# Performance work log

Hardware: AMD Instinct MI355X
Metric: run time of the kernel (lower is better)

Reference implementation:

```python
import jax, jax.numpy as jnp
import numpy as np

S, B, H = 2048, 2, 1024
NH = 16
HD = H // NH  # 64


def setup_inputs() -> dict:
    key = jax.random.key(0)
    k1, k2 = jax.random.split(key)
    hidden_states = jax.random.normal(k1, (S, B, H), dtype=jnp.float32)
    W_qkv = jax.random.normal(k2, (3 * H, H), dtype=jnp.float32) * (H ** -0.5)
    b_qkv = jnp.zeros((3 * H,), dtype=jnp.float32)
    return {"hidden_states": hidden_states, "W_qkv": W_qkv, "b_qkv": b_qkv}


def reference(hidden_states, W_qkv, b_qkv):
    s, b, h = hidden_states.shape
    # QKV projection: [S,B,3H] -> [S,B,NH,3*HD] -> split
    qkv = hidden_states @ W_qkv.T + b_qkv
    qkv = qkv.reshape(s, b, NH, 3 * HD)
    q, k, v = jnp.split(qkv, 3, axis=-1)  # each [S,B,NH,HD]
    norm_factor = HD ** -0.5
    # scores: [B,NH,Sq,Sk]
    scores = jnp.einsum('sbhd,tbhd->bhst', q, k) * norm_factor
    # Cumsum sequence-op (seq_op_in_fp32=True): cumsum over key dim, scaled by Sq^-0.5
    probs = jnp.cumsum(scores.astype(jnp.float32), axis=-1) * (s ** -0.5)
    probs = probs.astype(hidden_states.dtype)
    # PV: [B,NH,Sq,HD] -> seq-first [Sq,B,NH*HD]
    ctx = jnp.einsum('bhst,tbhd->sbhd', probs, v)
    return ctx.reshape(s, b, h)
```

## Files before the change

### kernel.cpp

```cpp
#include <hip/hip_runtime.h>

#define S 2048
#define B 2
#define H 1024
#define NH 16
#define HD 64
#define THREE_H 3072
#define ROWS (S*B)

typedef __attribute__((ext_vector_type(8))) short short8;
typedef __attribute__((ext_vector_type(4))) float f32x4;
typedef const __attribute__((address_space(1))) unsigned int* gptr_t;
typedef __attribute__((address_space(3))) unsigned int* lptr_t;

#define N8_A (ROWS * H / 8)
#define N8_W (THREE_H * H / 8)

__device__ __forceinline__ ushort f2bf(float f) {
    union { float f; unsigned u; } v; v.f = f;
    unsigned r = v.u + 0x7fffu + ((v.u >> 16) & 1u);
    return (ushort)(r >> 16);
}

__global__ void cast_both(const float* __restrict__ A, const float* __restrict__ W,
                          ushort* __restrict__ Ab, ushort* __restrict__ Wb) {
    int i = blockIdx.x * 256 + threadIdx.x;
    const float4* s4;
    ushort* dst;
    if (i < N8_A) { s4 = (const float4*)A; dst = Ab; }
    else if (i < N8_A + N8_W) { s4 = (const float4*)W; dst = Wb; i -= N8_A; }
    else return;
    float4 a = s4[2 * i], b = s4[2 * i + 1];
    short8 o;
    o[0] = f2bf(a.x); o[1] = f2bf(a.y); o[2] = f2bf(a.z); o[3] = f2bf(a.w);
    o[4] = f2bf(b.x); o[5] = f2bf(b.y); o[6] = f2bf(b.z); o[7] = f2bf(b.w);
    *(short8*)(dst + 8 * (size_t)i) = o;
}

__global__ __launch_bounds__(256) void qkv_gemm_mfma(const ushort* __restrict__ Abf,
                                                     const ushort* __restrict__ Wbf,
                                                     const float* __restrict__ bias,
                                                     ushort* __restrict__ Qb,
                                                     ushort* __restrict__ Kb,
                                                     float* __restrict__ Vf) {
    __shared__ ushort Abuf[128 * 32];
    __shared__ ushort Bbuf[128 * 32];
    const int tid = threadIdx.x;
    const int wave = tid >> 6, lane = tid & 63;
    const int wr = wave >> 1, wc = wave & 1;
    const int row0 = blockIdx.x * 128;
    const int col0 = blockIdx.y * 128;

    f32x4 acc[4][4] = {};

    const int lrow = lane >> 2;
    const int lk   = (lane & 3) * 8;

    for (int k0 = 0; k0 < H; k0 += 32) {
#pragma unroll
        for (int p = 0; p < 2; ++p) {
            int c = wave * 2 + p;
            int row = c * 16 + lrow;
            __builtin_amdgcn_global_load_lds(
                (gptr_t)&Abf[(size_t)(row0 + row) * H + k0 + lk],
                (lptr_t)&Abuf[c * 512 + lane * 8], 16, 0, 0);
            __builtin_amdgcn_global_load_lds(
                (gptr_t)&Wbf[(size_t)(col0 + row) * H + k0 + lk],
                (lptr_t)&Bbuf[c * 512 + lane * 8], 16, 0, 0);
        }
        __syncthreads();

        short8 af[4], bfr[4];
#pragma unroll
        for (int m = 0; m < 4; ++m) {
            int ar = wr * 64 + m * 16 + (lane & 15);
            af[m] = *(const short8*)&Abuf[ar * 32 + (lane >> 4) * 8];
            int br = wc * 64 + m * 16 + (lane & 15);
            bfr[m] = *(const short8*)&Bbuf[br * 32 + (lane >> 4) * 8];
        }
#pragma unroll
        for (int m = 0; m < 4; ++m)
#pragma unroll
            for (int n = 0; n < 4; ++n)
                acc[m][n] = __builtin_amdgcn_mfma_f32_16x16x32_bf16(af[m], bfr[n], acc[m][n], 0, 0, 0);
        __syncthreads();
    }

#pragma unroll
    for (int n = 0; n < 4; ++n) {
        int cbase = col0 + wc * 64 + n * 16;
        int h   = cbase / 192;
        int r3  = cbase % 192;
        int sel = r3 >> 6;
        int d   = (r3 & 63) + (lane & 15);
        float bv = bias[cbase + (lane & 15)];
#pragma unroll
        for (int m = 0; m < 4; ++m) {
            int rowb = row0 + wr * 64 + m * 16 + (lane >> 4) * 4;
#pragma unroll
            for (int j = 0; j < 4; ++j) {
                int r = rowb + j;
                int s = r >> 1, b = r & 1;
                size_t off = ((size_t)((b * NH + h) * S + s)) * HD + d;
                float val = acc[m][n][j] + bv;
                if (sel == 0)      Qb[off] = f2bf(val);
                else if (sel == 1) Kb[off] = f2bf(val);
                else               Vf[off] = val;
            }
        }
    }
}

__global__ void vsuf_chunksum(const float* __restrict__ Vf, float* __restrict__ csum) {
    int idx = blockIdx.x * 256 + threadIdx.x;
    int col = idx & 2047;
    int chunk = idx >> 11;
    const float* vp = Vf + ((size_t)(col >> 6) * S + chunk * 32) * HD + (col & 63);
    float s = 0.f;
#pragma unroll
    for (int t = 0; t < 32; ++t) s += vp[(size_t)t * HD];
    csum[idx] = s;
}

__global__ void vsuft_final(const float* __restrict__ Vf, const float* __restrict__ csum,
                            ushort* __restrict__ Vt) {
    int idx = blockIdx.x * 256 + threadIdx.x;
    int col = idx & 2047;
    int chunk = idx >> 11;
    int bh = col >> 6, d = col & 63;
    float acc = 0.f;
    for (int c = chunk + 1; c < 64; ++c) acc += csum[c * 2048 + col];
    const float* vp = Vf + ((size_t)bh * S + chunk * 32) * HD + d;
    ushort buf[32];
#pragma unroll
    for (int tt = 31; tt >= 0; --tt) {
        acc += vp[(size_t)tt * HD];
        buf[tt] = f2bf(acc);
    }
    ushort* op = Vt + ((size_t)bh * HD + d) * S + chunk * 32;
#pragma unroll
    for (int q = 0; q < 4; ++q) {
        short8 o;
#pragma unroll
        for (int k = 0; k < 8; ++k) o[k] = buf[q * 8 + k];
        *(short8*)(op + q * 8) = o;
    }
}

__global__ __launch_bounds__(256) void ktrans(const ushort* __restrict__ Kb,
                                              ushort* __restrict__ Kt) {
    __shared__ ushort Ks[64][72];
    const int bh = blockIdx.x;
    const int t0 = blockIdx.y * 64;
    const int tid = threadIdx.x;
    {
        const int tt = tid >> 2, part = (tid & 3) * 16;
        const ushort* src = Kb + ((size_t)bh * S + t0 + tt) * HD + part;
        *(short8*)&Ks[tt][part]     = *(const short8*)(src);
        *(short8*)&Ks[tt][part + 8] = *(const short8*)(src + 8);
    }
    __syncthreads();
    {
        const int d = tid >> 2, tq = (tid & 3) * 16;
        ushort tmp[16];
#pragma unroll
        for (int k = 0; k < 16; ++k) tmp[k] = Ks[tq + k][d];
        ushort* dst = Kt + ((size_t)bh * HD + d) * S + t0 + tq;
        short8 o0, o1;
#pragma unroll
        for (int k = 0; k < 8; ++k) { o0[k] = tmp[k]; o1[k] = tmp[8 + k]; }
        *(short8*)dst = o0;
        *(short8*)(dst + 8) = o1;
    }
}

__global__ __launch_bounds__(256) void kvm_mfma(const ushort* __restrict__ Kt,
                                                const ushort* __restrict__ Vt,
                                                float* __restrict__ Mpart) {
    const int bh = blockIdx.x, kb = blockIdx.y;
    const int tid = threadIdx.x, wave = tid >> 6, lane = tid & 63;
    const int slice = kb * 4 + wave;
    const ushort* Kp = Kt + (size_t)bh * HD * S;
    const ushort* Vp = Vt + (size_t)bh * HD * S;
    f32x4 acc[4][4] = {};
    const int il = lane & 15;
    const int tbase = slice * 128 + (lane >> 4) * 8;
#pragma unroll
    for (int ks = 0; ks < 4; ++ks) {
        const int t = tbase + ks * 32;
        short8 af[4], bfv[4];
#pragma unroll
        for (int m = 0; m < 4; ++m) af[m]  = *(const short8*)&Kp[(size_t)(m * 16 + il) * S + t];
#pragma unroll
        for (int n = 0; n < 4; ++n) bfv[n] = *(const short8*)&Vp[(size_t)(n * 16 + il) * S + t];
#pragma unroll
        for (int m = 0; m < 4; ++m)
#pragma unroll
            for (int n = 0; n < 4; ++n)
                acc[m][n] = __builtin_amdgcn_mfma_f32_16x16x32_bf16(af[m], bfv[n], acc[m][n], 0, 0, 0);
    }
    float* Mp = Mpart + ((size_t)slice * 32 + bh) * 4096;
#pragma unroll
    for (int m = 0; m < 4; ++m)
#pragma unroll
        for (int n = 0; n < 4; ++n)
#pragma unroll
            for (int j = 0; j < 4; ++j) {
                int i  = m * 16 + (lane >> 4) * 4 + j;
                int jj = n * 16 + il;
                Mp[i * 64 + jj] = acc[m][n][j];
            }
}

__global__ __launch_bounds__(256) void qm_mfma(const ushort* __restrict__ Qb,
                                               const float* __restrict__ Mpart,
                                               float* __restrict__ out) {
    __shared__ ushort Mt[64][72];
    const int bh = blockIdx.x, b = bh >> 4, h = bh & 15;
    const int tid = threadIdx.x;
    {
        const int i = tid >> 2, jq = (tid & 3) * 16;
        f32x4 s0 = {}, s1 = {}, s2 = {}, s3 = {};
#pragma unroll
        for (int sl = 0; sl < 16; ++sl) {
            const float* p = Mpart + ((size_t)sl * 32 + bh) * 4096 + i * 64 + jq;
            s0 += *(const f32x4*)(p);
            s1 += *(const f32x4*)(p + 4);
            s2 += *(const f32x4*)(p + 8);
            s3 += *(const f32x4*)(p + 12);
        }
#pragma unroll
        for (int k = 0; k < 4; ++k) {
            Mt[jq + 0  + k][i] = f2bf(s0[k]);
            Mt[jq + 4  + k][i] = f2bf(s1[k]);
            Mt[jq + 8  + k][i] = f2bf(s2[k]);
            Mt[jq + 12 + k][i] = f2bf(s3[k]);
        }
    }
    __syncthreads();
    const int wave = tid >> 6, lane = tid & 63;
    const int sl15 = lane & 15, koct = (lane >> 4) * 8;
    const int s0b = blockIdx.y * 256 + wave * 64;
    f32x4 acc[4][4] = {};
#pragma unroll
    for (int ks = 0; ks < 2; ++ks) {
        short8 af[4], bfv[4];
#pragma unroll
        for (int m = 0; m < 4; ++m) {
            int s = s0b + m * 16 + sl15;
            af[m] = *(const short8*)&Qb[((size_t)bh * S + s) * HD + ks * 32 + koct];
        }
#pragma unroll
        for (int n = 0; n < 4; ++n)
            bfv[n] = *(const short8*)&Mt[n * 16 + sl15][ks * 32 + koct];
#pragma unroll
        for (int m = 0; m < 4; ++m)
#pragma unroll
            for (int n = 0; n < 4; ++n)
                acc[m][n] = __builtin_amdgcn_mfma_f32_16x16x32_bf16(af[m], bfv[n], acc[m][n], 0, 0, 0);
    }
    const float scale = 0.125f * 0.02209708691207961f;
#pragma unroll
    for (int m = 0; m < 4; ++m)
#pragma unroll
        for (int n = 0; n < 4; ++n)
#pragma unroll
            for (int j = 0; j < 4; ++j) {
                int s = s0b + m * 16 + (lane >> 4) * 4 + j;
                int d = n * 16 + sl15;
                out[(size_t)(s * B + b) * H + h * 64 + d] = acc[m][n][j] * scale;
            }
}

extern "C" void kernel_launch(void* const* d_in, const int* in_sizes, int n_in,
                              void* d_out, int out_size, void* d_ws, size_t ws_size,
                              hipStream_t stream) {
    const float* hidden = (const float*)d_in[0];
    const float* W      = (const float*)d_in[1];
    const float* bias   = (const float*)d_in[2];
    float* out = (float*)d_out;

    float*  Vf    = (float*)d_ws;
    ushort* Qb    = (ushort*)(Vf + 4194304);
    ushort* Kb    = Qb + 4194304;
    ushort* Kt    = Kb + 4194304;
    ushort* Vt    = Kt + 4194304;
    float*  csum  = (float*)(Vt + 4194304);
    float*  Mpart = csum + 131072;
    ushort* Abf   = (ushort*)(Mpart + 2097152);
    ushort* Wbf   = Abf + 4194304;

    cast_both<<<(N8_A + N8_W + 255) / 256, 256, 0, stream>>>(hidden, W, Abf, Wbf);
    qkv_gemm_mfma<<<dim3(ROWS / 128, THREE_H / 128), 256, 0, stream>>>(Abf, Wbf, bias, Qb, Kb, Vf);
    vsuf_chunksum<<<512, 256, 0, stream>>>(Vf, csum);
    vsuft_final<<<512, 256, 0, stream>>>(Vf, csum, Vt);
    ktrans<<<dim3(32, 32), 256, 0, stream>>>(Kb, Kt);
    kvm_mfma<<<dim3(32, 4), 256, 0, stream>>>(Kt, Vt, Mpart);
    qm_mfma<<<dim3(32, 8), 256, 0, stream>>>(Qb, Mpart, out);
}
```

Measured before the change: 86.16 us.

## Fuse K/V transpose into QKV GEMM epilogue and keep V in bf16

```diff
diff --git a/kernel.cpp b/kernel.cpp
--- a/kernel.cpp
+++ b/kernel.cpp
@@ -20,6 +20,10 @@
     union { float f; unsigned u; } v; v.f = f;
     unsigned r = v.u + 0x7fffu + ((v.u >> 16) & 1u);
     return (ushort)(r >> 16);
+}
+__device__ __forceinline__ float bf2f(ushort u) {
+    union { unsigned u; float f; } v; v.u = ((unsigned)u) << 16;
+    return v.f;
 }
 
 __global__ void cast_both(const float* __restrict__ A, const float* __restrict__ W,
@@ -41,10 +45,11 @@
                                                      const ushort* __restrict__ Wbf,
                                                      const float* __restrict__ bias,
                                                      ushort* __restrict__ Qb,
-                                                     ushort* __restrict__ Kb,
-                                                     float* __restrict__ Vf) {
+                                                     ushort* __restrict__ Kt,
+                                                     ushort* __restrict__ Vraw) {
     __shared__ ushort Abuf[128 * 32];
     __shared__ ushort Bbuf[128 * 32];
+    __shared__ ushort Ct[64][136];
     const int tid = threadIdx.x;
     const int wave = tid >> 6, lane = tid & 63;
     const int wr = wave >> 1, wc = wave & 1;
@@ -86,91 +91,102 @@
         __syncthreads();
     }
 
-#pragma unroll
-    for (int n = 0; n < 4; ++n) {
-        int cbase = col0 + wc * 64 + n * 16;
-        int h   = cbase / 192;
-        int r3  = cbase % 192;
-        int sel = r3 >> 6;
-        int d   = (r3 & 63) + (lane & 15);
-        float bv = bias[cbase + (lane & 15)];
-#pragma unroll
-        for (int m = 0; m < 4; ++m) {
-            int rowb = row0 + wr * 64 + m * 16 + (lane >> 4) * 4;
-#pragma unroll
-            for (int j = 0; j < 4; ++j) {
-                int r = rowb + j;
-                int s = r >> 1, b = r & 1;
-                size_t off = ((size_t)((b * NH + h) * S + s)) * HD + d;
-                float val = acc[m][n][j] + bv;
-                if (sel == 0)      Qb[off] = f2bf(val);
-                else if (sel == 1) Kb[off] = f2bf(val);
-                else               Vf[off] = val;
-            }
-        }
-    }
-}
-
-__global__ void vsuf_chunksum(const float* __restrict__ Vf, float* __restrict__ csum) {
+    const int il = lane & 15, g = lane >> 4;
+    const int t_base = row0 >> 1;
+#pragma unroll
+    for (int sg = 0; sg < 2; ++sg) {
+        int cseg = col0 + sg * 64;
+        int h = cseg / 192, rem = cseg % 192;
+        int sel = rem >> 6;
+        if (sel == 0) {
+            if (wc == sg) {
+#pragma unroll
+                for (int n = 0; n < 4; ++n) {
+                    int d = n * 16 + il;
+                    float bv = bias[cseg + d];
+#pragma unroll
+                    for (int m = 0; m < 4; ++m) {
+                        int rowb = row0 + wr * 64 + m * 16 + g * 4;
+#pragma unroll
+                        for (int j = 0; j < 4; ++j) {
+                            int r = rowb + j;
+                            int s = r >> 1, b = r & 1;
+                            Qb[((size_t)((b * NH + h) * S + s)) * HD + d] =
+                                f2bf(acc[m][n][j] + bv);
+                        }
+                    }
+                }
+            }
+        } else {
+            ushort* dst = (sel == 1) ? Kt : Vraw;
+            __syncthreads();
+            if (wc == sg) {
+#pragma unroll
+                for (int n = 0; n < 4; ++n) {
+                    int c = n * 16 + il;
+                    float bv = bias[cseg + c];
+#pragma unroll
+                    for (int m = 0; m < 4; ++m) {
+                        int t0 = wr * 32 + m * 8 + g * 2;
+                        uint lo = (uint)f2bf(acc[m][n][0] + bv) |
+                                  ((uint)f2bf(acc[m][n][2] + bv) << 16);
+                        uint hi = (uint)f2bf(acc[m][n][1] + bv) |
+                                  ((uint)f2bf(acc[m][n][3] + bv) << 16);
+                        *(uint*)&Ct[c][t0]      = lo;
+                        *(uint*)&Ct[c][64 + t0] = hi;
+                    }
+                }
+            }
+            __syncthreads();
+            {
+                int c = tid >> 2, sub = tid & 3, b = sub >> 1, th = (sub & 1) * 32;
+                ushort* op = dst + ((size_t)((b * NH + h) * HD + c)) * S + t_base + th;
+                const ushort* sp = &Ct[c][b * 64 + th];
+#pragma unroll
+                for (int q = 0; q < 4; ++q)
+                    *(short8*)(op + q * 8) = *(const short8*)(sp + q * 8);
+            }
+        }
+    }
+}
+
+__global__ void vsuf_chunksum(const ushort* __restrict__ Vraw, float* __restrict__ csum) {
     int idx = blockIdx.x * 256 + threadIdx.x;
     int col = idx & 2047;
     int chunk = idx >> 11;
-    const float* vp = Vf + ((size_t)(col >> 6) * S + chunk * 32) * HD + (col & 63);
+    const ushort* vp = Vraw + (size_t)col * S + chunk * 32;
     float s = 0.f;
 #pragma unroll
-    for (int t = 0; t < 32; ++t) s += vp[(size_t)t * HD];
-    csum[idx] = s;
-}
-
-__global__ void vsuft_final(const float* __restrict__ Vf, const float* __restrict__ csum,
-                            ushort* __restrict__ Vt) {
+    for (int q = 0; q < 4; ++q) {
+        short8 v = *(const short8*)(vp + q * 8);
+#pragma unroll
+        for (int k = 0; k < 8; ++k) s += bf2f((ushort)v[k]);
+    }
+    csum[chunk * 2048 + col] = s;
+}
+
+__global__ void vsuf_final(ushort* __restrict__ Vraw, const float* __restrict__ csum) {
     int idx = blockIdx.x * 256 + threadIdx.x;
     int col = idx & 2047;
     int chunk = idx >> 11;
-    int bh = col >> 6, d = col & 63;
     float acc = 0.f;
     for (int c = chunk + 1; c < 64; ++c) acc += csum[c * 2048 + col];
-    const float* vp = Vf + ((size_t)bh * S + chunk * 32) * HD + d;
-    ushort buf[32];
-#pragma unroll
-    for (int tt = 31; tt >= 0; --tt) {
-        acc += vp[(size_t)tt * HD];
-        buf[tt] = f2bf(acc);
-    }
-    ushort* op = Vt + ((size_t)bh * HD + d) * S + chunk * 32;
+    ushort* vp = Vraw + (size_t)col * S + chunk * 32;
+    float v[32];
+#pragma unroll
+    for (int q = 0; q < 4; ++q) {
+        short8 x = *(const short8*)(vp + q * 8);
+#pragma unroll
+        for (int k = 0; k < 8; ++k) v[q * 8 + k] = bf2f((ushort)x[k]);
+    }
+#pragma unroll
+    for (int tt = 31; tt >= 0; --tt) { acc += v[tt]; v[tt] = acc; }
 #pragma unroll
     for (int q = 0; q < 4; ++q) {
         short8 o;
 #pragma unroll
-        for (int k = 0; k < 8; ++k) o[k] = buf[q * 8 + k];
-        *(short8*)(op + q * 8) = o;
-    }
-}
-
-__global__ __launch_bounds__(256) void ktrans(const ushort* __restrict__ Kb,
-                                              ushort* __restrict__ Kt) {
-    __shared__ ushort Ks[64][72];
-    const int bh = blockIdx.x;
-    const int t0 = blockIdx.y * 64;
-    const int tid = threadIdx.x;
-    {
-        const int tt = tid >> 2, part = (tid & 3) * 16;
-        const ushort* src = Kb + ((size_t)bh * S + t0 + tt) * HD + part;
-        *(short8*)&Ks[tt][part]     = *(const short8*)(src);
-        *(short8*)&Ks[tt][part + 8] = *(const short8*)(src + 8);
-    }
-    __syncthreads();
-    {
-        const int d = tid >> 2, tq = (tid & 3) * 16;
-        ushort tmp[16];
-#pragma unroll
-        for (int k = 0; k < 16; ++k) tmp[k] = Ks[tq + k][d];
-        ushort* dst = Kt + ((size_t)bh * HD + d) * S + t0 + tq;
-        short8 o0, o1;
-#pragma unroll
-        for (int k = 0; k < 8; ++k) { o0[k] = tmp[k]; o1[k] = tmp[8 + k]; }
-        *(short8*)dst = o0;
-        *(short8*)(dst + 8) = o1;
+        for (int k = 0; k < 8; ++k) o[k] = f2bf(v[q * 8 + k]);
+        *(short8*)(vp + q * 8) = o;
     }
 }
 
@@ -280,21 +296,18 @@
     const float* bias   = (const float*)d_in[2];
     float* out = (float*)d_out;
 
-    float*  Vf    = (float*)d_ws;
-    ushort* Qb    = (ushort*)(Vf + 4194304);
-    ushort* Kb    = Qb + 4194304;
-    ushort* Kt    = Kb + 4194304;
-    ushort* Vt    = Kt + 4194304;
-    float*  csum  = (float*)(Vt + 4194304);
+    ushort* Qb    = (ushort*)d_ws;
+    ushort* Kt    = Qb + 4194304;
+    ushort* Vraw  = Kt + 4194304;
+    float*  csum  = (float*)(Vraw + 4194304);
     float*  Mpart = csum + 131072;
     ushort* Abf   = (ushort*)(Mpart + 2097152);
     ushort* Wbf   = Abf + 4194304;
 
     cast_both<<<(N8_A + N8_W + 255) / 256, 256, 0, stream>>>(hidden, W, Abf, Wbf);
-    qkv_gemm_mfma<<<dim3(ROWS / 128, THREE_H / 128), 256, 0, stream>>>(Abf, Wbf, bias, Qb, Kb, Vf);
-    vsuf_chunksum<<<512, 256, 0, stream>>>(Vf, csum);
-    vsuft_final<<<512, 256, 0, stream>>>(Vf, csum, Vt);
-    ktrans<<<dim3(32, 32), 256, 0, stream>>>(Kb, Kt);
-    kvm_mfma<<<dim3(32, 4), 256, 0, stream>>>(Kt, Vt, Mpart);
+    qkv_gemm_mfma<<<dim3(ROWS / 128, THREE_H / 128), 256, 0, stream>>>(Abf, Wbf, bias, Qb, Kt, Vraw);
+    vsuf_chunksum<<<512, 256, 0, stream>>>(Vraw, csum);
+    vsuf_final<<<512, 256, 0, stream>>>(Vraw, csum);
+    kvm_mfma<<<dim3(32, 4), 256, 0, stream>>>(Kt, Vraw, Mpart);
     qm_mfma<<<dim3(32, 8), 256, 0, stream>>>(Qb, Mpart, out);
 }
```

Result: slower. 92.04 us (+6.8%).
